# Performance work log

Measured on AMD Instinct MI355X. Metric: run time of the kernel, lower is better.

Reference implementation:

```python
import jax, jax.numpy as jnp
import numpy as np

K = 7  # kernel_size
D = 2  # dilation


def window_start(idx, L, K, D):
    """NATTEN neighborhood window start (clamped at borders, dilation-group aware)."""
    nh = K // 2
    if D <= 1:
        return jnp.maximum(idx - nh, 0) + jnp.where(idx + nh >= L, L - idx - nh - 1, 0)
    ni = idx - nh * D
    imodd = idx % D
    a = (L // D) * D
    b = L - a
    right = jnp.where(imodd < b, L - b + imodd - 2 * nh * D, a + imodd - K * D)
    return jnp.where(ni < 0, imodd, jnp.where(idx + nh * D >= L, right, ni))


def setup_inputs() -> dict:
    key = jax.random.key(0)
    ks = jax.random.split(key, 7)
    B, Cin, H, W, Cout = 2, 128, 112, 112, 64
    x = jax.random.normal(ks[0], (B, Cin, H, W), dtype=jnp.float32)
    Wq = jax.random.normal(ks[1], (Cout, Cin), dtype=jnp.float32) * 0.02
    Wk = jax.random.normal(ks[2], (Cout, Cin), dtype=jnp.float32) * 0.02
    Wv = jax.random.normal(ks[3], (Cout, Cin), dtype=jnp.float32) * 0.02
    bq = jax.random.normal(ks[4], (Cout,), dtype=jnp.float32) * 0.02
    bk = jax.random.normal(ks[5], (Cout,), dtype=jnp.float32) * 0.02
    bv = jax.random.normal(ks[6], (Cout,), dtype=jnp.float32) * 0.02
    return {"x": x, "Wq": Wq, "bq": bq, "Wk": Wk, "bk": bk, "Wv": Wv, "bv": bv}


def reference(x, Wq, bq, Wk, bk, Wv, bv):
    B, Cin, H, W = x.shape
    # 1x1 conv projections -> channels-last [B, H, W, C]
    q = jnp.einsum('bchw,oc->bhwo', x, Wq) + bq
    k = jnp.einsum('bchw,oc->bhwo', x, Wk) + bk
    v = jnp.einsum('bchw,oc->bhwo', x, Wv) + bv
    C = q.shape[-1]
    scale = jnp.asarray(C, q.dtype) ** -0.5  # NATTEN default scale (heads=1, head_dim=C)

    offs = jnp.arange(K) * D
    ih = window_start(jnp.arange(H), H, K, D)[:, None] + offs  # [H, K]
    iw = window_start(jnp.arange(W), W, K, D)[:, None] + offs  # [W, K]
    # gather neighborhoods -> [B, H, W, K, K, C]
    idx_h = ih[:, None, :, None]  # [H,1,K,1]
    idx_w = iw[None, :, None, :]  # [1,W,1,K]
    kw = k[:, idx_h, idx_w, :]
    vw = v[:, idx_h, idx_w, :]

    scores = jnp.einsum('bhwc,bhwijc->bhwij', q * scale, kw)  # [B,H,W,K,K]
    attn = jax.nn.softmax(scores.reshape(B, H, W, K * K), axis=-1)
    out = jnp.einsum('bhwn,bhwnc->bhwc', attn, vw.reshape(B, H, W, K * K, C))
    return out.transpose(0, 3, 1, 2)  # [B, C, H, W]
```

## Files before the change

kernel.cpp:

```cpp
#include <hip/hip_runtime.h>
#include <hip/hip_bf16.h>

#define HWSZ 12544
#define WDIM 112
#define CIN  128
#define NPIX 25088
#define VPITCH 68

typedef __attribute__((ext_vector_type(8))) short          short8;
typedef __attribute__((ext_vector_type(4))) float          float4v;
typedef __attribute__((ext_vector_type(4))) unsigned short ushort4v;

__device__ __forceinline__ int window_start7x2(int idx, int L) {
    int ni = idx - 6;
    int imodd = idx & 1;
    int a = (L >> 1) << 1;
    int bb = L - a;
    int right = (imodd < bb) ? (L - bb + imodd - 12) : (a + imodd - 14);
    if (ni < 0) return imodd;
    if (idx + 6 >= L) return right;
    return ni;
}

__device__ __forceinline__ unsigned short f2bf(float f) {
    __hip_bfloat16 h = __float2bfloat16(f);
    return *(unsigned short*)&h;
}
__device__ __forceinline__ float bf2f(unsigned short u) {
    __hip_bfloat16 h = *(__hip_bfloat16*)&u;
    return __bfloat162float(h);
}

__global__ __launch_bounds__(256) void proj_mfma(
    const float* __restrict__ x,
    const float* __restrict__ Wq, const float* __restrict__ bq,
    const float* __restrict__ Wk, const float* __restrict__ bk,
    const float* __restrict__ Wv, const float* __restrict__ bv,
    unsigned short* __restrict__ qkv)
{
    __shared__ __align__(16) unsigned short wsb[64][136];

    const int t = threadIdx.x, lane = t & 63, wv = t >> 6, quad = lane >> 4;
    const int m = blockIdx.y;
    const float* Wm = (m == 0) ? Wq : (m == 1) ? Wk : Wv;
    const float* bm = (m == 0) ? bq : (m == 1) ? bk : bv;
    unsigned short* outm = qkv + (size_t)m * NPIX * 64;

    const int pix0 = blockIdx.x * 64;
    const int b    = pix0 / HWSZ;
    const int hw0  = pix0 - b * HWSZ;
    const float* xb = x + (size_t)b * CIN * HWSZ;

    #pragma unroll
    for (int i = 0; i < 8; ++i) {
        int u = t + 256 * i;
        int o = u >> 5, cq = (u & 31) * 4;
        float4 w4 = *(const float4*)&Wm[o * 128 + cq];
        ushort4v s4 = { f2bf(w4.x), f2bf(w4.y), f2bf(w4.z), f2bf(w4.w) };
        *(ushort4v*)&wsb[o][cq] = s4;
    }

    const int hwpx = hw0 + wv * 16 + (lane & 15);
    short8 af[4];
    #pragma unroll
    for (int kc = 0; kc < 4; ++kc) {
        #pragma unroll
        for (int j = 0; j < 8; ++j) {
            int c = kc * 32 + quad * 8 + j;
            af[kc][j] = (short)f2bf(xb[(size_t)c * HWSZ + hwpx]);
        }
    }
    __syncthreads();

    float4v acc[4] = {{0,0,0,0},{0,0,0,0},{0,0,0,0},{0,0,0,0}};
    #pragma unroll
    for (int kc = 0; kc < 4; ++kc) {
        #pragma unroll
        for (int nt = 0; nt < 4; ++nt) {
            short8 bf = *(const short8*)&wsb[nt * 16 + (lane & 15)][kc * 32 + quad * 8];
            acc[nt] = __builtin_amdgcn_mfma_f32_16x16x32_bf16(af[kc], bf, acc[nt], 0, 0, 0);
        }
    }

    const float scale = (m == 0) ? 0.125f : 1.0f;
    #pragma unroll
    for (int nt = 0; nt < 4; ++nt) {
        int o = nt * 16 + (lane & 15);
        float bias = bm[o];
        #pragma unroll
        for (int r = 0; r < 4; ++r) {
            int px = wv * 16 + quad * 4 + r;
            outm[(size_t)(pix0 + px) * 64 + o] = f2bf((acc[r==r?nt:nt][r] + bias) * scale);
        }
    }
}

__global__ __launch_bounds__(256) void attn_mfma(
    const unsigned short* __restrict__ qkv, float* __restrict__ out)
{
    __shared__ __align__(16) unsigned short vsn[160 * VPITCH];
    __shared__ __align__(16) unsigned short ps[16 * 168];

    const int t = threadIdx.x, lane = t & 63, wv = t >> 6, quad = lane >> 4;
    const int bx  = blockIdx.x;
    const int b   = bx / 896;  const int rem = bx - b * 896;
    const int h   = rem >> 3;  const int sub = rem & 7;
    const int g   = sub & 1;
    const int pbi = sub >> 1;
    const int pb  = (pbi < 3) ? pbi * 16 : 40;

    const int hs  = window_start7x2(h, WDIM);
    const int ws0 = window_start7x2(2 * pb + g, WDIM);
    const int pixbase = b * HWSZ;

    const unsigned short* qg = qkv;
    const unsigned short* kg = qkv + (size_t)NPIX * 64;
    const unsigned short* vg = qkv + 2 * (size_t)NPIX * 64;

    for (int u = t; u < 154 * 16; u += 256) {
        int key = u >> 4, cc = (u & 15) * 4;
        int i = (unsigned)key / 22u, c = key - i * 22;
        int kw = ws0 + 2 * c; if (kw > 111) kw = 111;
        int kp = pixbase + (hs + 2 * i) * WDIM + kw;
        *(ushort4v*)&vsn[key * VPITCH + cc] =
            *(const ushort4v*)(vg + (size_t)kp * 64 + cc);
    }
    for (int u = t; u < 6 * VPITCH; u += 256) vsn[154 * VPITCH + u] = 0;

    const int qpix = pixbase + h * WDIM + 2 * (pb + (lane & 15)) + g;
    short8 af[2];
    #pragma unroll
    for (int kc = 0; kc < 2; ++kc)
        af[kc] = *(const short8*)(qg + (size_t)qpix * 64 + kc * 32 + quad * 8);

    int cb_r[4];
    #pragma unroll
    for (int r = 0; r < 4; ++r) {
        int px = quad * 4 + r;
        cb_r[r] = (window_start7x2(2 * (pb + px) + g, WDIM) - ws0) >> 1;
    }

    for (int nt = wv; nt < 10; nt += 4) {
        int keyb = nt * 16 + (lane & 15);
        int i = (unsigned)keyb / 22u, c = keyb - i * 22;
        int kw = ws0 + 2 * c; if (kw > 111) kw = 111;
        int kp = pixbase + (hs + 2 * i) * WDIM + kw;
        float4v acc = {0,0,0,0};
        #pragma unroll
        for (int kc = 0; kc < 2; ++kc) {
            short8 bf = *(const short8*)(kg + (size_t)kp * 64 + kc * 32 + quad * 8);
            acc = __builtin_amdgcn_mfma_f32_16x16x32_bf16(af[kc], bf, acc, 0, 0, 0);
        }
        bool colok = (keyb < 154);
        #pragma unroll
        for (int r = 0; r < 4; ++r) {
            bool valid = colok && ((unsigned)(c - cb_r[r]) < 7u);
            float sv = valid ? acc[r] : -1e30f;
            int px = quad * 4 + r;
            ps[px * 168 + keyb] = f2bf(sv);
        }
    }
    __syncthreads();

    {
        const int row = t >> 4, slot = t & 15;
        float sv[10]; float mx = -1e30f;
        #pragma unroll
        for (int k2 = 0; k2 < 10; ++k2) {
            sv[k2] = bf2f(ps[row * 168 + slot + 16 * k2]);
            mx = fmaxf(mx, sv[k2]);
        }
        #pragma unroll
        for (int msk = 1; msk < 16; msk <<= 1)
            mx = fmaxf(mx, __shfl_xor(mx, msk, 64));
        float sum = 0.0f;
        #pragma unroll
        for (int k2 = 0; k2 < 10; ++k2) {
            sv[k2] = __expf(sv[k2] - mx);
            sum += sv[k2];
        }
        #pragma unroll
        for (int msk = 1; msk < 16; msk <<= 1)
            sum += __shfl_xor(sum, msk, 64);
        float rinv = 1.0f / sum;
        #pragma unroll
        for (int k2 = 0; k2 < 10; ++k2)
            ps[row * 168 + slot + 16 * k2] = f2bf(sv[k2] * rinv);
    }
    __syncthreads();

    const int ch = wv * 16 + (lane & 15);
    float4v oacc = {0,0,0,0};
    #pragma unroll
    for (int kc = 0; kc < 5; ++kc) {
        short8 pa = *(const short8*)&ps[(lane & 15) * 168 + kc * 32 + quad * 8];
        short8 vb;
        int kbase = (kc * 32 + quad * 8) * VPITCH + ch;
        #pragma unroll
        for (int j = 0; j < 8; ++j)
            vb[j] = (short)vsn[kbase + j * VPITCH];
        oacc = __builtin_amdgcn_mfma_f32_16x16x32_bf16(pa, vb, oacc, 0, 0, 0);
    }
    {
        float* ob = out + (size_t)(b * 64 + ch) * HWSZ + h * WDIM;
        #pragma unroll
        for (int r = 0; r < 4; ++r) {
            int px = quad * 4 + r;
            ob[2 * (pb + px) + g] = oacc[r];
        }
    }
}

extern "C" void kernel_launch(void* const* d_in, const int* in_sizes, int n_in,
                              void* d_out, int out_size, void* d_ws, size_t ws_size,
                              hipStream_t stream) {
    const float* x  = (const float*)d_in[0];
    const float* Wq = (const float*)d_in[1];
    const float* bq = (const float*)d_in[2];
    const float* Wk = (const float*)d_in[3];
    const float* bk = (const float*)d_in[4];
    const float* Wv = (const float*)d_in[5];
    const float* bv = (const float*)d_in[6];
    float* out = (float*)d_out;

    unsigned short* qkv = (unsigned short*)d_ws;

    proj_mfma<<<dim3(392, 3), dim3(256), 0, stream>>>(x, Wq, bq, Wk, bk, Wv, bv, qkv);
    attn_mfma<<<dim3(1792), dim3(256), 0, stream>>>(qkv, out);
}
```

Baseline: 96.92 us.

## Fuse QKV projections per block and read V directly from global memory

The projection kernel now computes Q, K and V for each 64-pixel tile in a single block. It stages all three weight matrices in shared memory, so x is read once instead of three times. The attention kernel drops the V shared-memory staging and instead gathers V values straight from global memory inside the P·V MFMA loop, with per-element address computation. This saves LDS traffic and the staging pass, at the cost of scattered 2-byte global loads and more integer arithmetic per element. Out-of-range keys are redirected to a safe address, where they are masked by zero probabilities.

```diff
diff --git a/kernel.cpp b/kernel.cpp
--- a/kernel.cpp
+++ b/kernel.cpp
@@ -5,7 +5,6 @@
 #define WDIM 112
 #define CIN  128
 #define NPIX 25088
-#define VPITCH 68
 
 typedef __attribute__((ext_vector_type(8))) short          short8;
 typedef __attribute__((ext_vector_type(4))) float          float4v;
@@ -38,26 +37,25 @@
     const float* __restrict__ Wv, const float* __restrict__ bv,
     unsigned short* __restrict__ qkv)
 {
-    __shared__ __align__(16) unsigned short wsb[64][136];
+    __shared__ __align__(16) unsigned short wsb[3][64][136];
 
     const int t = threadIdx.x, lane = t & 63, wv = t >> 6, quad = lane >> 4;
-    const int m = blockIdx.y;
-    const float* Wm = (m == 0) ? Wq : (m == 1) ? Wk : Wv;
-    const float* bm = (m == 0) ? bq : (m == 1) ? bk : bv;
-    unsigned short* outm = qkv + (size_t)m * NPIX * 64;
 
     const int pix0 = blockIdx.x * 64;
     const int b    = pix0 / HWSZ;
     const int hw0  = pix0 - b * HWSZ;
     const float* xb = x + (size_t)b * CIN * HWSZ;
 
-    #pragma unroll
-    for (int i = 0; i < 8; ++i) {
-        int u = t + 256 * i;
-        int o = u >> 5, cq = (u & 31) * 4;
-        float4 w4 = *(const float4*)&Wm[o * 128 + cq];
+    const float* Ws[3] = {Wq, Wk, Wv};
+    #pragma unroll
+    for (int i = 0; i < 24; ++i) {
+        int u   = i * 256 + t;
+        int m   = u >> 11;
+        int rem = u & 2047;
+        int o = rem >> 5, cq = (rem & 31) * 4;
+        float4 w4 = *(const float4*)&Ws[m][o * 128 + cq];
         ushort4v s4 = { f2bf(w4.x), f2bf(w4.y), f2bf(w4.z), f2bf(w4.w) };
-        *(ushort4v*)&wsb[o][cq] = s4;
+        *(ushort4v*)&wsb[m][o][cq] = s4;
     }
 
     const int hwpx = hw0 + wv * 16 + (lane & 15);
@@ -72,25 +70,29 @@
     }
     __syncthreads();
 
-    float4v acc[4] = {{0,0,0,0},{0,0,0,0},{0,0,0,0},{0,0,0,0}};
-    #pragma unroll
-    for (int kc = 0; kc < 4; ++kc) {
+    const float* bs[3] = {bq, bk, bv};
+    #pragma unroll
+    for (int m = 0; m < 3; ++m) {
+        float4v acc[4] = {{0,0,0,0},{0,0,0,0},{0,0,0,0},{0,0,0,0}};
+        #pragma unroll
+        for (int kc = 0; kc < 4; ++kc) {
+            #pragma unroll
+            for (int nt = 0; nt < 4; ++nt) {
+                short8 bf = *(const short8*)&wsb[m][nt * 16 + (lane & 15)][kc * 32 + quad * 8];
+                acc[nt] = __builtin_amdgcn_mfma_f32_16x16x32_bf16(af[kc], bf, acc[nt], 0, 0, 0);
+            }
+        }
+        const float scale = (m == 0) ? 0.125f : 1.0f;
+        unsigned short* outm = qkv + (size_t)m * NPIX * 64;
         #pragma unroll
         for (int nt = 0; nt < 4; ++nt) {
-            short8 bf = *(const short8*)&wsb[nt * 16 + (lane & 15)][kc * 32 + quad * 8];
-            acc[nt] = __builtin_amdgcn_mfma_f32_16x16x32_bf16(af[kc], bf, acc[nt], 0, 0, 0);
-        }
-    }
-
-    const float scale = (m == 0) ? 0.125f : 1.0f;
-    #pragma unroll
-    for (int nt = 0; nt < 4; ++nt) {
-        int o = nt * 16 + (lane & 15);
-        float bias = bm[o];
-        #pragma unroll
-        for (int r = 0; r < 4; ++r) {
-            int px = wv * 16 + quad * 4 + r;
-            outm[(size_t)(pix0 + px) * 64 + o] = f2bf((acc[r==r?nt:nt][r] + bias) * scale);
+            int o = nt * 16 + (lane & 15);
+            float bias = bs[m][o];
+            #pragma unroll
+            for (int r = 0; r < 4; ++r) {
+                int px = wv * 16 + quad * 4 + r;
+                outm[(size_t)(pix0 + px) * 64 + o] = f2bf((acc[nt][r] + bias) * scale);
+            }
         }
     }
 }
@@ -98,7 +100,6 @@
 __global__ __launch_bounds__(256) void attn_mfma(
     const unsigned short* __restrict__ qkv, float* __restrict__ out)
 {
-    __shared__ __align__(16) unsigned short vsn[160 * VPITCH];
     __shared__ __align__(16) unsigned short ps[16 * 168];
 
     const int t = threadIdx.x, lane = t & 63, wv = t >> 6, quad = lane >> 4;
@@ -117,16 +118,6 @@
     const unsigned short* kg = qkv + (size_t)NPIX * 64;
     const unsigned short* vg = qkv + 2 * (size_t)NPIX * 64;
 
-    for (int u = t; u < 154 * 16; u += 256) {
-        int key = u >> 4, cc = (u & 15) * 4;
-        int i = (unsigned)key / 22u, c = key - i * 22;
-        int kw = ws0 + 2 * c; if (kw > 111) kw = 111;
-        int kp = pixbase + (hs + 2 * i) * WDIM + kw;
-        *(ushort4v*)&vsn[key * VPITCH + cc] =
-            *(const ushort4v*)(vg + (size_t)kp * 64 + cc);
-    }
-    for (int u = t; u < 6 * VPITCH; u += 256) vsn[154 * VPITCH + u] = 0;
-
     const int qpix = pixbase + h * WDIM + 2 * (pb + (lane & 15)) + g;
     short8 af[2];
     #pragma unroll
@@ -145,6 +136,7 @@
         int i = (unsigned)keyb / 22u, c = keyb - i * 22;
         int kw = ws0 + 2 * c; if (kw > 111) kw = 111;
         int kp = pixbase + (hs + 2 * i) * WDIM + kw;
+        if (keyb >= 154) kp = pixbase;
         float4v acc = {0,0,0,0};
         #pragma unroll
         for (int kc = 0; kc < 2; ++kc) {
@@ -195,10 +187,14 @@
     for (int kc = 0; kc < 5; ++kc) {
         short8 pa = *(const short8*)&ps[(lane & 15) * 168 + kc * 32 + quad * 8];
         short8 vb;
-        int kbase = (kc * 32 + quad * 8) * VPITCH + ch;
-        #pragma unroll
-        for (int j = 0; j < 8; ++j)
-            vb[j] = (short)vsn[kbase + j * VPITCH];
+        #pragma unroll
+        for (int j = 0; j < 8; ++j) {
+            int key = kc * 32 + quad * 8 + j;
+            int i = (unsigned)key / 22u, c = key - i * 22;
+            int kw = ws0 + 2 * c; if (kw > 111) kw = 111;
+            int kp = (key < 154) ? (pixbase + (hs + 2 * i) * WDIM + kw) : pixbase;
+            vb[j] = (short)vg[(size_t)kp * 64 + ch];
+        }
         oacc = __builtin_amdgcn_mfma_f32_16x16x32_bf16(pa, vb, oacc, 0, 0, 0);
     }
     {
@@ -225,6 +221,6 @@
 
     unsigned short* qkv = (unsigned short*)d_ws;
 
-    proj_mfma<<<dim3(392, 3), dim3(256), 0, stream>>>(x, Wq, bq, Wk, bk, Wv, bv, qkv);
+    proj_mfma<<<dim3(392), dim3(256), 0, stream>>>(x, Wq, bq, Wk, bk, Wv, bv, qkv);
     attn_mfma<<<dim3(1792), dim3(256), 0, stream>>>(qkv, out);
 }
```

Result: slower. 101.0 us (+4.2%).

## Store V channel-major by column parity and run attention as single-wave blocks

Applied to the files above, without the earlier changes.

The projection kernel now writes V transposed into a [batch, parity, channel, h*56+w/2] layout. The attention kernel can then load V fragments straight from global memory as contiguous 8-element vectors, with no LDS staging or strided LDS gathers. The attention kernel shrinks to one 64-thread wave per block. Scores stay in registers across 14 key tiles covering 32-aligned window columns, and the query scale moves from the projection into the score computation. This removes block-wide syncs and the V shared-memory copy, in exchange for more redundant key MFMAs over padded columns, higher register pressure, and scattered 2-byte stores when writing the transposed V.

```diff
diff --git a/kernel.cpp b/kernel.cpp
--- a/kernel.cpp
+++ b/kernel.cpp
@@ -5,7 +5,7 @@
 #define WDIM 112
 #define CIN  128
 #define NPIX 25088
-#define VPITCH 68
+#define VTROW 6272
 
 typedef __attribute__((ext_vector_type(8))) short          short8;
 typedef __attribute__((ext_vector_type(4))) float          float4v;
@@ -26,17 +26,13 @@
     __hip_bfloat16 h = __float2bfloat16(f);
     return *(unsigned short*)&h;
 }
-__device__ __forceinline__ float bf2f(unsigned short u) {
-    __hip_bfloat16 h = *(__hip_bfloat16*)&u;
-    return __bfloat162float(h);
-}
 
 __global__ __launch_bounds__(256) void proj_mfma(
     const float* __restrict__ x,
     const float* __restrict__ Wq, const float* __restrict__ bq,
     const float* __restrict__ Wk, const float* __restrict__ bk,
     const float* __restrict__ Wv, const float* __restrict__ bv,
-    unsigned short* __restrict__ qkv)
+    unsigned short* __restrict__ qbuf)
 {
     __shared__ __align__(16) unsigned short wsb[64][136];
 
@@ -44,10 +40,9 @@
     const int m = blockIdx.y;
     const float* Wm = (m == 0) ? Wq : (m == 1) ? Wk : Wv;
     const float* bm = (m == 0) ? bq : (m == 1) ? bk : bv;
-    unsigned short* outm = qkv + (size_t)m * NPIX * 64;
 
     const int pix0 = blockIdx.x * 64;
-    const int b    = pix0 / HWSZ;
+    const int b    = blockIdx.x / 196;
     const int hw0  = pix0 - b * HWSZ;
     const float* xb = x + (size_t)b * CIN * HWSZ;
 
@@ -82,26 +77,43 @@
         }
     }
 
-    const float scale = (m == 0) ? 0.125f : 1.0f;
-    #pragma unroll
-    for (int nt = 0; nt < 4; ++nt) {
-        int o = nt * 16 + (lane & 15);
-        float bias = bm[o];
-        #pragma unroll
-        for (int r = 0; r < 4; ++r) {
-            int px = wv * 16 + quad * 4 + r;
-            outm[(size_t)(pix0 + px) * 64 + o] = f2bf((acc[r==r?nt:nt][r] + bias) * scale);
-        }
-    }
-}
-
-__global__ __launch_bounds__(256) void attn_mfma(
+    if (m < 2) {
+        const float scale = (m == 0) ? 0.125f : 1.0f;
+        unsigned short* outm = qbuf + (size_t)m * NPIX * 64;
+        #pragma unroll
+        for (int nt = 0; nt < 4; ++nt) {
+            int o = nt * 16 + (lane & 15);
+            float bias = bm[o];
+            #pragma unroll
+            for (int r = 0; r < 4; ++r) {
+                int px = wv * 16 + quad * 4 + r;
+                outm[(size_t)(pix0 + px) * 64 + o] = f2bf(acc[nt][r] + bias);
+            }
+        }
+    } else {
+        unsigned short* vt = qbuf + 2 * (size_t)NPIX * 64;
+        #pragma unroll
+        for (int nt = 0; nt < 4; ++nt) {
+            int ch = nt * 16 + (lane & 15);
+            float bias = bm[ch];
+            #pragma unroll
+            for (int r = 0; r < 4; ++r) {
+                int hw = hw0 + wv * 16 + quad * 4 + r;
+                int h2 = (unsigned)hw / 112u;
+                int w  = hw - h2 * 112;
+                vt[(size_t)((b * 2 + (w & 1)) * 64 + ch) * VTROW + h2 * 56 + (w >> 1)]
+                    = f2bf(acc[nt][r] + bias);
+            }
+        }
+    }
+}
+
+__global__ __launch_bounds__(64) void attn_mfma(
     const unsigned short* __restrict__ qkv, float* __restrict__ out)
 {
-    __shared__ __align__(16) unsigned short vsn[160 * VPITCH];
-    __shared__ __align__(16) unsigned short ps[16 * 168];
-
-    const int t = threadIdx.x, lane = t & 63, wv = t >> 6, quad = lane >> 4;
+    __shared__ __align__(16) unsigned short ps[16 * 232];
+
+    const int lane = threadIdx.x, quad = lane >> 4, col = lane & 15;
     const int bx  = blockIdx.x;
     const int b   = bx / 896;  const int rem = bx - b * 896;
     const int h   = rem >> 3;  const int sub = rem & 7;
@@ -111,103 +123,90 @@
 
     const int hs  = window_start7x2(h, WDIM);
     const int ws0 = window_start7x2(2 * pb + g, WDIM);
+    const int cb0 = (ws0 >> 1) & ~7;
     const int pixbase = b * HWSZ;
 
     const unsigned short* qg = qkv;
     const unsigned short* kg = qkv + (size_t)NPIX * 64;
-    const unsigned short* vg = qkv + 2 * (size_t)NPIX * 64;
-
-    for (int u = t; u < 154 * 16; u += 256) {
-        int key = u >> 4, cc = (u & 15) * 4;
-        int i = (unsigned)key / 22u, c = key - i * 22;
-        int kw = ws0 + 2 * c; if (kw > 111) kw = 111;
+    const unsigned short* vt = qkv + 2 * (size_t)NPIX * 64
+                             + (size_t)(b * 2 + g) * 64 * VTROW;
+
+    const int qpix = pixbase + h * WDIM + 2 * (pb + col) + g;
+    short8 af0 = *(const short8*)(qg + (size_t)qpix * 64 + quad * 8);
+    short8 af1 = *(const short8*)(qg + (size_t)qpix * 64 + 32 + quad * 8);
+
+    int cbr[4];
+    #pragma unroll
+    for (int r = 0; r < 4; ++r)
+        cbr[r] = (window_start7x2(2 * (pb + quad * 4 + r) + g, WDIM) >> 1) - cb0;
+
+    float4v S[14];
+    #pragma unroll
+    for (int nt = 0; nt < 14; ++nt) {
+        int u = nt * 16 + col;
+        int i = u >> 5, c = u & 31;
+        int wcol = cb0 + c;
+        int kw = 2 * wcol + g; kw = (kw > 111) ? 111 : kw;
         int kp = pixbase + (hs + 2 * i) * WDIM + kw;
-        *(ushort4v*)&vsn[key * VPITCH + cc] =
-            *(const ushort4v*)(vg + (size_t)kp * 64 + cc);
-    }
-    for (int u = t; u < 6 * VPITCH; u += 256) vsn[154 * VPITCH + u] = 0;
-
-    const int qpix = pixbase + h * WDIM + 2 * (pb + (lane & 15)) + g;
-    short8 af[2];
-    #pragma unroll
-    for (int kc = 0; kc < 2; ++kc)
-        af[kc] = *(const short8*)(qg + (size_t)qpix * 64 + kc * 32 + quad * 8);
-
-    int cb_r[4];
+        float4v a = {0, 0, 0, 0};
+        a = __builtin_amdgcn_mfma_f32_16x16x32_bf16(
+                af0, *(const short8*)(kg + (size_t)kp * 64 + quad * 8), a, 0, 0, 0);
+        a = __builtin_amdgcn_mfma_f32_16x16x32_bf16(
+                af1, *(const short8*)(kg + (size_t)kp * 64 + 32 + quad * 8), a, 0, 0, 0);
+        bool colok = (wcol <= 55);
+        #pragma unroll
+        for (int r = 0; r < 4; ++r) {
+            bool valid = colok && ((unsigned)(c - cbr[r]) < 7u);
+            S[nt][r] = valid ? a[r] * 0.125f : -1e30f;
+        }
+    }
+
     #pragma unroll
     for (int r = 0; r < 4; ++r) {
-        int px = quad * 4 + r;
-        cb_r[r] = (window_start7x2(2 * (pb + px) + g, WDIM) - ws0) >> 1;
-    }
-
-    for (int nt = wv; nt < 10; nt += 4) {
-        int keyb = nt * 16 + (lane & 15);
-        int i = (unsigned)keyb / 22u, c = keyb - i * 22;
-        int kw = ws0 + 2 * c; if (kw > 111) kw = 111;
-        int kp = pixbase + (hs + 2 * i) * WDIM + kw;
-        float4v acc = {0,0,0,0};
-        #pragma unroll
-        for (int kc = 0; kc < 2; ++kc) {
-            short8 bf = *(const short8*)(kg + (size_t)kp * 64 + kc * 32 + quad * 8);
-            acc = __builtin_amdgcn_mfma_f32_16x16x32_bf16(af[kc], bf, acc, 0, 0, 0);
-        }
-        bool colok = (keyb < 154);
-        #pragma unroll
-        for (int r = 0; r < 4; ++r) {
-            bool valid = colok && ((unsigned)(c - cb_r[r]) < 7u);
-            float sv = valid ? acc[r] : -1e30f;
-            int px = quad * 4 + r;
-            ps[px * 168 + keyb] = f2bf(sv);
-        }
-    }
-    __syncthreads();
-
-    {
-        const int row = t >> 4, slot = t & 15;
-        float sv[10]; float mx = -1e30f;
-        #pragma unroll
-        for (int k2 = 0; k2 < 10; ++k2) {
-            sv[k2] = bf2f(ps[row * 168 + slot + 16 * k2]);
-            mx = fmaxf(mx, sv[k2]);
-        }
+        float mx = S[0][r];
+        #pragma unroll
+        for (int nt = 1; nt < 14; ++nt) mx = fmaxf(mx, S[nt][r]);
         #pragma unroll
         for (int msk = 1; msk < 16; msk <<= 1)
             mx = fmaxf(mx, __shfl_xor(mx, msk, 64));
         float sum = 0.0f;
         #pragma unroll
-        for (int k2 = 0; k2 < 10; ++k2) {
-            sv[k2] = __expf(sv[k2] - mx);
-            sum += sv[k2];
+        for (int nt = 0; nt < 14; ++nt) {
+            float e = __expf(S[nt][r] - mx);
+            S[nt][r] = e;
+            sum += e;
         }
         #pragma unroll
         for (int msk = 1; msk < 16; msk <<= 1)
             sum += __shfl_xor(sum, msk, 64);
         float rinv = 1.0f / sum;
-        #pragma unroll
-        for (int k2 = 0; k2 < 10; ++k2)
-            ps[row * 168 + slot + 16 * k2] = f2bf(sv[k2] * rinv);
-    }
-    __syncthreads();
-
-    const int ch = wv * 16 + (lane & 15);
-    float4v oacc = {0,0,0,0};
-    #pragma unroll
-    for (int kc = 0; kc < 5; ++kc) {
-        short8 pa = *(const short8*)&ps[(lane & 15) * 168 + kc * 32 + quad * 8];
-        short8 vb;
-        int kbase = (kc * 32 + quad * 8) * VPITCH + ch;
-        #pragma unroll
-        for (int j = 0; j < 8; ++j)
-            vb[j] = (short)vsn[kbase + j * VPITCH];
-        oacc = __builtin_amdgcn_mfma_f32_16x16x32_bf16(pa, vb, oacc, 0, 0, 0);
-    }
-    {
+        int row = quad * 4 + r;
+        #pragma unroll
+        for (int nt = 0; nt < 14; ++nt)
+            ps[row * 232 + nt * 16 + col] = f2bf(S[nt][r] * rinv);
+    }
+
+    float4v O[4] = {{0,0,0,0},{0,0,0,0},{0,0,0,0},{0,0,0,0}};
+    #pragma unroll
+    for (int kc = 0; kc < 7; ++kc) {
+        short8 pa = *(const short8*)&ps[col * 232 + kc * 32 + quad * 8];
+        int u8 = kc * 32 + quad * 8;
+        int i = u8 >> 5, c0 = u8 & 31;
+        int rowoff = (hs + 2 * i) * 56 + cb0 + c0;
+        #pragma unroll
+        for (int nt = 0; nt < 4; ++nt) {
+            short8 vb = *(const short8*)(vt + (size_t)(nt * 16 + col) * VTROW + rowoff);
+            O[nt] = __builtin_amdgcn_mfma_f32_16x16x32_bf16(pa, vb, O[nt], 0, 0, 0);
+        }
+    }
+
+    #pragma unroll
+    for (int nt = 0; nt < 4; ++nt) {
+        int ch = nt * 16 + col;
         float* ob = out + (size_t)(b * 64 + ch) * HWSZ + h * WDIM;
         #pragma unroll
-        for (int r = 0; r < 4; ++r) {
-            int px = quad * 4 + r;
-            ob[2 * (pb + px) + g] = oacc[r];
-        }
+        for (int r = 0; r < 4; ++r)
+            ob[2 * (pb + quad * 4 + r) + g] = O[nt][r];
     }
 }
 
@@ -226,5 +225,5 @@
     unsigned short* qkv = (unsigned short*)d_ws;
 
     proj_mfma<<<dim3(392, 3), dim3(256), 0, stream>>>(x, Wq, bq, Wk, bk, Wv, bv, qkv);
-    attn_mfma<<<dim3(1792), dim3(256), 0, stream>>>(qkv, out);
-}
+    attn_mfma<<<dim3(1792), dim3(64), 0, stream>>>(qkv, out);
+}
```

New measurement: 99.90 us. +3.1%, slower.
